# Performance work log

Hardware: AMD Instinct MI355X
Metric: run time of the kernel (lower is better)

## Reference

```python
import jax, jax.numpy as jnp
import numpy as np

N = 100_000
E = 1_000_000
F_IN = 128
F_OUT = 64
NHOP = 2


def _xavier(k, shape, gain=1.414):
    fan_in, fan_out = shape
    std = gain * np.sqrt(2.0 / (fan_in + fan_out))
    return (jax.random.normal(k, shape) * std).astype(jnp.float32)


def setup_inputs() -> dict:
    key = jax.random.key(0)
    ks = jax.random.split(key, 8)
    x = jax.random.normal(ks[0], (N, F_IN), jnp.float32)
    edge_index = jax.random.randint(ks[1], (2, E), 0, N)
    edge_attr = jax.random.uniform(ks[2], (E,), jnp.float32)
    W0 = _xavier(ks[3], (F_IN, F_OUT))
    W1 = _xavier(ks[4], (F_IN, F_OUT))
    b0 = jnp.zeros((F_OUT,), jnp.float32)
    b1 = jnp.zeros((F_OUT,), jnp.float32)
    fc0 = _xavier(ks[5], (F_OUT, 1))
    fc1 = _xavier(ks[6], (F_OUT, 1))
    bf0 = jnp.zeros((1,), jnp.float32)
    bf1 = jnp.zeros((1,), jnp.float32)
    return dict(x=x, edge_index=edge_index, edge_attr=edge_attr,
                W0=W0, b0=b0, W1=W1, b1=b1,
                fc0=fc0, bf0=bf0, fc1=fc1, bf1=bf1)


def _spmm(row, col, val, v, n):
    # (A v)[r] = sum over edges (r -> c) of val * v[c]
    return jax.ops.segment_sum(val[:, None] * v[col], row, num_segments=n)


def _adaptive_enc(y, fc, bf):
    # NodeAdaptiveEncoder (eval mode): relu(y) + sigmoid(y@fc+bf) * min(y, 0)
    g = jax.nn.sigmoid(y @ fc + bf)  # [N, 1]
    return jnp.where(y < 0, 0.0, y) + g * jnp.where(y > 0, 0.0, y)


def reference(x, edge_index, edge_attr, W0, b0, W1, b1, fc0, bf0, fc1, bf1):
    n = x.shape[0]
    row, col = edge_index[0], edge_index[1]
    ones = jnp.ones((n, 1), x.dtype)
    params = [(W0, b0, fc0, bf0), (W1, b1, fc1, bf1)]
    outs = []
    for hop in range(NHOP):
        W, b, fc, bf = params[hop]
        h = x @ W  # [N, F_OUT]
        # identity attention; row_uniform norm of A^(hop+1) factors as
        # (A^(hop+1) h) / (A^(hop+1) 1) -- exact since spspmm sums duplicates.
        agg, deg = h, ones
        for _ in range(hop + 1):
            agg = _spmm(row, col, edge_attr, agg, n)
            deg = _spmm(row, col, edge_attr, deg, n)
        safe_deg = jnp.where(deg > 0, deg, 1.0)
        y = jnp.where(deg > 0, agg / safe_deg, 0.0)  # NaN mask for empty rows
        y = y + b
        outs.append(_adaptive_enc(y, fc, bf))
    return jnp.concatenate(outs, axis=1)  # [N, NHOP * F_OUT]
```

## Files before the change

### kernel.cpp

```cpp
#include <hip/hip_runtime.h>

#define F_IN 128
#define F_ALL 128
#define F_HOP 64

#define RPB_BITS 8
#define RPB 256
#define KB_MAX 512
#define NBLK_BIN 256
#define ECAP 3072

typedef unsigned int uint;
typedef unsigned short ushort;
typedef __attribute__((ext_vector_type(8))) short short8v;
typedef __attribute__((ext_vector_type(4))) float float4v;

__device__ __forceinline__ uint pack_bf16(float lo, float hi) {
    uint ul = __float_as_uint(lo), uh = __float_as_uint(hi);
    ul += 0x7FFFu + ((ul >> 16) & 1u);
    uh += 0x7FFFu + ((uh >> 16) & 1u);
    return (ul >> 16) | (uh & 0xFFFF0000u);
}
__device__ __forceinline__ float bf_lo(uint h) { return __uint_as_float(h << 16); }
__device__ __forceinline__ float bf_hi(uint h) { return __uint_as_float(h & 0xFFFF0000u); }

__global__ __launch_bounds__(256) void gemm_hist_kernel(
    const float* __restrict__ x, const float* __restrict__ W0,
    const float* __restrict__ W1, uint* __restrict__ H2,
    const int* __restrict__ ei, int* __restrict__ bhist,
    int N, int E, int K, int gemmBlocks) {
    __shared__ ushort Wlds[16384];

    if ((int)blockIdx.x >= gemmBlocks) {
        int* h = (int*)Wlds;
        const int hb = blockIdx.x - gemmBlocks;
        for (int i = threadIdx.x; i < K; i += 256) h[i] = 0;
        __syncthreads();
        const int chunk = (E + NBLK_BIN - 1) / NBLK_BIN;
        const int s = hb * chunk;
        const int e = min(s + chunk, E);
        for (int j = s + threadIdx.x; j < e; j += 256)
            atomicAdd(&h[__builtin_nontemporal_load(ei + j) >> RPB_BITS], 1);
        __syncthreads();
        for (int i = threadIdx.x; i < K; i += 256)
            bhist[hb * KB_MAX + i] = h[i];
        return;
    }

    {
        const int t = threadIdx.x;
        #pragma unroll
        for (int i = 0; i < 8; ++i) {
            const int e    = t + 256 * i;
            const int lane = e & 63;
            const int tile = e >> 6;
            const int kt   = tile >> 3;
            const int nt   = tile & 7;
            const int k0   = kt * 32 + (lane >> 4) * 8;
            const int n    = nt * 16 + (lane & 15);
            const float* src = (n < 64) ? (W0 + n) : (W1 + (n - 64));
            float v[8];
            #pragma unroll
            for (int j = 0; j < 8; ++j) v[j] = src[(size_t)(k0 + j) * F_HOP];
            uint4 o;
            o.x = pack_bf16(v[0], v[1]);
            o.y = pack_bf16(v[2], v[3]);
            o.z = pack_bf16(v[4], v[5]);
            o.w = pack_bf16(v[6], v[7]);
            *((uint4*)Wlds + e) = o;
        }
    }
    __syncthreads();

    const int wv   = threadIdx.x >> 6;
    const int lane = threadIdx.x & 63;
    const int rbase = blockIdx.x * 64 + wv * 16;
    if (rbase >= N) return;

    const int m    = lane & 15;
    const int quad = lane >> 4;
    const float* xrow = x + (size_t)(rbase + m) * F_IN + quad * 8;

    float4v acc[8];
    #pragma unroll
    for (int t = 0; t < 8; ++t) acc[t] = (float4v){0.f, 0.f, 0.f, 0.f};

    #pragma unroll
    for (int kt = 0; kt < 4; ++kt) {
        const float4v xa = __builtin_nontemporal_load((const float4v*)(xrow + kt * 32));
        const float4v xb = __builtin_nontemporal_load((const float4v*)(xrow + kt * 32 + 4));
        union { uint4 u; short8v s; } av;
        av.u.x = pack_bf16(xa[0], xa[1]);
        av.u.y = pack_bf16(xa[2], xa[3]);
        av.u.z = pack_bf16(xb[0], xb[1]);
        av.u.w = pack_bf16(xb[2], xb[3]);
        #pragma unroll
        for (int nt = 0; nt < 8; ++nt) {
            union { uint4 u; short8v s; } bv;
            bv.u = *((const uint4*)Wlds + (kt * 8 + nt) * 64 + lane);
            acc[nt] = __builtin_amdgcn_mfma_f32_16x16x32_bf16(av.s, bv.s, acc[nt], 0, 0, 0);
        }
    }

    #pragma unroll
    for (int t = 0; t < 4; ++t) {
        #pragma unroll
        for (int i = 0; i < 4; ++i) {
            const int r = rbase + quad * 4 + i;
            H2[(size_t)r * F_HOP + t * 16 + m] = pack_bf16(acc[t][i], acc[t + 4][i]);
        }
    }
}

__global__ __launch_bounds__(256) void blockscan_kernel(
    int* __restrict__ bhist, int* __restrict__ btot,
    int* __restrict__ rowptr, int E, int N) {
    __shared__ int wsum[4];
    const int b = blockIdx.x;
    const int t = threadIdx.x;
    const int s = bhist[t * KB_MAX + b];
    int v = s;
    #pragma unroll
    for (int d = 1; d < 64; d <<= 1) {
        int u = __shfl_up(v, (unsigned)d, 64);
        if ((t & 63) >= d) v += u;
    }
    if ((t & 63) == 63) wsum[t >> 6] = v;
    __syncthreads();
    int off = 0;
    #pragma unroll
    for (int i = 0; i < 4; ++i) if (i < (t >> 6)) off += wsum[i];
    bhist[t * KB_MAX + b] = off + v - s;
    if (t == 255) btot[b] = off + v;
    if (b == 0 && t == 0) rowptr[N] = E;
}

__global__ __launch_bounds__(256) void bin_kernel(
    const int* __restrict__ ei, const float* __restrict__ ea,
    const int* __restrict__ bloc, const int* __restrict__ btot,
    int2* __restrict__ gbuf, int E, int K) {
    __shared__ int bb[KB_MAX];
    __shared__ int cur[KB_MAX];
    __shared__ int wsum[4];
    const int t = threadIdx.x;
    const int i0 = 2 * t, i1 = 2 * t + 1;
    const int c0 = (i0 < K) ? btot[i0] : 0;
    const int c1 = (i1 < K) ? btot[i1] : 0;
    const int s = c0 + c1;
    int v = s;
    #pragma unroll
    for (int d = 1; d < 64; d <<= 1) {
        int u = __shfl_up(v, (unsigned)d, 64);
        if ((t & 63) >= d) v += u;
    }
    if ((t & 63) == 63) wsum[t >> 6] = v;
    __syncthreads();
    {
        int off = 0;
        #pragma unroll
        for (int i = 0; i < 4; ++i) if (i < (t >> 6)) off += wsum[i];
        const int excl = off + v - s;
        if (i0 < K) bb[i0] = excl;
        if (i1 < K) bb[i1] = excl + c0;
    }
    __syncthreads();
    for (int i = t; i < K; i += 256)
        cur[i] = bb[i] + bloc[blockIdx.x * KB_MAX + i];
    __syncthreads();
    const int chunk = (E + NBLK_BIN - 1) / NBLK_BIN;
    const int s0 = blockIdx.x * chunk;
    const int e0 = min(s0 + chunk, E);
    for (int j = s0 + t; j < e0; j += 256) {
        const int r = __builtin_nontemporal_load(ei + j);
        const int c = __builtin_nontemporal_load(ei + E + j);
        const int vv = __float_as_int(__builtin_nontemporal_load(ea + j));
        const int b = r >> RPB_BITS;
        const int gp = atomicAdd(&cur[b], 1);
        gbuf[gp] = make_int2(c | ((r & (RPB - 1)) << 17), vv);
    }
}

__global__ __launch_bounds__(512) void sort_kernel(
    const int* __restrict__ btot, const int2* __restrict__ gbuf,
    int2* __restrict__ ecv, int* __restrict__ rowptr, int E, int K, int N) {
    __shared__ int2 ebuf[ECAP];
    __shared__ int cnt[RPB];
    __shared__ int bb[KB_MAX + 1];
    __shared__ int wsum[4];
    const int b = blockIdx.x;
    const int t = threadIdx.x;
    const int i0 = 2 * t, i1 = 2 * t + 1;
    const int c0 = (t < 256 && i0 < K) ? btot[i0] : 0;
    const int c1 = (t < 256 && i1 < K) ? btot[i1] : 0;
    const int s = c0 + c1;
    int v = s;
    #pragma unroll
    for (int d = 1; d < 64; d <<= 1) {
        int u = __shfl_up(v, (unsigned)d, 64);
        if ((t & 63) >= d) v += u;
    }
    if (t < 256 && (t & 63) == 63) wsum[t >> 6] = v;
    if (t < RPB) cnt[t] = 0;
    __syncthreads();
    if (t < 256) {
        int off = 0;
        #pragma unroll
        for (int i = 0; i < 4; ++i) if (i < (t >> 6)) off += wsum[i];
        const int excl = off + v - s;
        if (i0 < K) bb[i0] = excl;
        if (i1 < K) bb[i1] = excl + c0;
    }
    if (t == 0) bb[K] = E;
    __syncthreads();
    const int bstart = bb[b], bend = bb[b + 1];
    const int m = bend - bstart;
    const int row0 = b << RPB_BITS;
    for (int j = t; j < m; j += 512) {
        const int2 p = gbuf[bstart + j];
        if (j < ECAP) ebuf[j] = p;
        atomicAdd(&cnt[(p.x >> 17) & (RPB - 1)], 1);
    }
    __syncthreads();
    const int s2 = (t < 256) ? cnt[t] : 0;
    int v2 = s2;
    #pragma unroll
    for (int d = 1; d < 64; d <<= 1) {
        int u = __shfl_up(v2, (unsigned)d, 64);
        if ((t & 63) >= d) v2 += u;
    }
    if (t < 256 && (t & 63) == 63) wsum[t >> 6] = v2;
    __syncthreads();
    int excl2 = 0;
    if (t < 256) {
        int off = 0;
        #pragma unroll
        for (int i = 0; i < 4; ++i) if (i < (t >> 6)) off += wsum[i];
        excl2 = off + v2 - s2;
        const int r0 = row0 + t;
        if (r0 < N) rowptr[r0] = bstart + excl2;
    }
    __syncthreads();
    if (t < 256) cnt[t] = excl2;
    __syncthreads();
    for (int j = t; j < m; j += 512) {
        const int2 p = (j < ECAP) ? ebuf[j] : gbuf[bstart + j];
        const int lr = (p.x >> 17) & (RPB - 1);
        const int pos = atomicAdd(&cnt[lr], 1);
        ecv[bstart + pos] = make_int2(p.x & 0x1FFFF, p.y);
    }
}

__global__ __launch_bounds__(256) void pass1_kernel(
    const int* __restrict__ rowptr, const int2* __restrict__ ecv,
    const uint* __restrict__ H2,
    const float* __restrict__ b0, const float* __restrict__ fc0,
    const float* __restrict__ bf0,
    float* __restrict__ out, ushort* __restrict__ T16,
    float* __restrict__ dg1, int N) {
    const int lane = threadIdx.x & 63;
    const int g    = lane >> 4;
    const int l    = lane & 15;
    const int r = blockIdx.x * 16 + (threadIdx.x >> 6) * 4 + g;
    if (r >= N) return;
    const int f0 = l * 4;
    const uint* __restrict__ H2b = H2 + f0;
    const int jb = rowptr[r], je = rowptr[r + 1];

    float s00 = 0.f, s01 = 0.f, s02 = 0.f, s03 = 0.f;
    float s10 = 0.f, s11 = 0.f, s12 = 0.f, s13 = 0.f;
    float d = 0.f;
    int j = jb;
    for (; j + 4 <= je; j += 4) {
        const int2 e0 = ecv[j], e1 = ecv[j + 1], e2 = ecv[j + 2], e3 = ecv[j + 3];
        const uint4 h0 = *(const uint4*)(H2b + (size_t)e0.x * F_HOP);
        const uint4 h1 = *(const uint4*)(H2b + (size_t)e1.x * F_HOP);
        const uint4 h2 = *(const uint4*)(H2b + (size_t)e2.x * F_HOP);
        const uint4 h3 = *(const uint4*)(H2b + (size_t)e3.x * F_HOP);
        const float v0 = __int_as_float(e0.y), v1 = __int_as_float(e1.y);
        const float v2 = __int_as_float(e2.y), v3 = __int_as_float(e3.y);
        d += (v0 + v1) + (v2 + v3);
        s00 = fmaf(v0, bf_lo(h0.x), s00); s10 = fmaf(v0, bf_hi(h0.x), s10);
        s01 = fmaf(v0, bf_lo(h0.y), s01); s11 = fmaf(v0, bf_hi(h0.y), s11);
        s02 = fmaf(v0, bf_lo(h0.z), s02); s12 = fmaf(v0, bf_hi(h0.z), s12);
        s03 = fmaf(v0, bf_lo(h0.w), s03); s13 = fmaf(v0, bf_hi(h0.w), s13);
        s00 = fmaf(v1, bf_lo(h1.x), s00); s10 = fmaf(v1, bf_hi(h1.x), s10);
        s01 = fmaf(v1, bf_lo(h1.y), s01); s11 = fmaf(v1, bf_hi(h1.y), s11);
        s02 = fmaf(v1, bf_lo(h1.z), s02); s12 = fmaf(v1, bf_hi(h1.z), s12);
        s03 = fmaf(v1, bf_lo(h1.w), s03); s13 = fmaf(v1, bf_hi(h1.w), s13);
        s00 = fmaf(v2, bf_lo(h2.x), s00); s10 = fmaf(v2, bf_hi(h2.x), s10);
        s01 = fmaf(v2, bf_lo(h2.y), s01); s11 = fmaf(v2, bf_hi(h2.y), s11);
        s02 = fmaf(v2, bf_lo(h2.z), s02); s12 = fmaf(v2, bf_hi(h2.z), s12);
        s03 = fmaf(v2, bf_lo(h2.w), s03); s13 = fmaf(v2, bf_hi(h2.w), s13);
        s00 = fmaf(v3, bf_lo(h3.x), s00); s10 = fmaf(v3, bf_hi(h3.x), s10);
        s01 = fmaf(v3, bf_lo(h3.y), s01); s11 = fmaf(v3, bf_hi(h3.y), s11);
        s02 = fmaf(v3, bf_lo(h3.z), s02); s12 = fmaf(v3, bf_hi(h3.z), s12);
        s03 = fmaf(v3, bf_lo(h3.w), s03); s13 = fmaf(v3, bf_hi(h3.w), s13);
    }
    for (; j < je; ++j) {
        const int2 e0 = ecv[j];
        const uint4 h0 = *(const uint4*)(H2b + (size_t)e0.x * F_HOP);
        const float v0 = __int_as_float(e0.y);
        d += v0;
        s00 = fmaf(v0, bf_lo(h0.x), s00); s10 = fmaf(v0, bf_hi(h0.x), s10);
        s01 = fmaf(v0, bf_lo(h0.y), s01); s11 = fmaf(v0, bf_hi(h0.y), s11);
        s02 = fmaf(v0, bf_lo(h0.z), s02); s12 = fmaf(v0, bf_hi(h0.z), s12);
        s03 = fmaf(v0, bf_lo(h0.w), s03); s13 = fmaf(v0, bf_hi(h0.w), s13);
    }

    uint2 tw;
    tw.x = pack_bf16(s10, s11);
    tw.y = pack_bf16(s12, s13);
    *(uint2*)(T16 + (size_t)r * F_HOP + f0) = tw;
    if (l == 0) dg1[r] = d;

    const float inv = (d > 0.f) ? 1.f / d : 0.f;
    const float4 bb = *(const float4*)(b0 + f0);
    const float4 ff = *(const float4*)(fc0 + f0);
    const float y0 = s00 * inv + bb.x;
    const float y1 = s01 * inv + bb.y;
    const float y2 = s02 * inv + bb.z;
    const float y3 = s03 * inv + bb.w;
    float t = y0 * ff.x + y1 * ff.y + y2 * ff.z + y3 * ff.w;
    #pragma unroll
    for (int m = 1; m < 16; m <<= 1) t += __shfl_xor(t, m, 64);
    const float gg = 1.f / (1.f + __expf(-(t + bf0[0])));
    float4v o;
    o[0] = fmaxf(y0, 0.f) + gg * fminf(y0, 0.f);
    o[1] = fmaxf(y1, 0.f) + gg * fminf(y1, 0.f);
    o[2] = fmaxf(y2, 0.f) + gg * fminf(y2, 0.f);
    o[3] = fmaxf(y3, 0.f) + gg * fminf(y3, 0.f);
    __builtin_nontemporal_store(o, (float4v*)(out + (size_t)r * F_ALL + f0));
}

__global__ __launch_bounds__(256) void pass2_kernel(
    const int* __restrict__ rowptr, const int2* __restrict__ ecv,
    const ushort* __restrict__ T16, const float* __restrict__ dg1,
    const float* __restrict__ b1, const float* __restrict__ fc1,
    const float* __restrict__ bf1,
    float* __restrict__ out, int N) {
    const int lane = threadIdx.x & 63;
    const int g    = lane >> 4;
    const int l    = lane & 15;
    const int r = blockIdx.x * 16 + (threadIdx.x >> 6) * 4 + g;
    if (r >= N) return;
    const int f0 = l * 4;
    const ushort* __restrict__ Tb = T16 + f0;
    const int jb = rowptr[r], je = rowptr[r + 1];

    float s0 = 0.f, s1 = 0.f, s2 = 0.f, s3 = 0.f;
    float d2 = 0.f;
    int j = jb;
    for (; j + 4 <= je; j += 4) {
        const int2 e0 = ecv[j], e1 = ecv[j + 1], e2 = ecv[j + 2], e3 = ecv[j + 3];
        const uint2 t0 = *(const uint2*)(Tb + (size_t)e0.x * F_HOP);
        const uint2 t1 = *(const uint2*)(Tb + (size_t)e1.x * F_HOP);
        const uint2 t2 = *(const uint2*)(Tb + (size_t)e2.x * F_HOP);
        const uint2 t3 = *(const uint2*)(Tb + (size_t)e3.x * F_HOP);
        const float g0 = dg1[e0.x], g1 = dg1[e1.x], g2 = dg1[e2.x], g3 = dg1[e3.x];
        const float v0 = __int_as_float(e0.y), v1 = __int_as_float(e1.y);
        const float v2 = __int_as_float(e2.y), v3 = __int_as_float(e3.y);
        d2 = fmaf(v0, g0, d2); d2 = fmaf(v1, g1, d2);
        d2 = fmaf(v2, g2, d2); d2 = fmaf(v3, g3, d2);
        s0 = fmaf(v0, bf_lo(t0.x), s0); s1 = fmaf(v0, bf_hi(t0.x), s1);
        s2 = fmaf(v0, bf_lo(t0.y), s2); s3 = fmaf(v0, bf_hi(t0.y), s3);
        s0 = fmaf(v1, bf_lo(t1.x), s0); s1 = fmaf(v1, bf_hi(t1.x), s1);
        s2 = fmaf(v1, bf_lo(t1.y), s2); s3 = fmaf(v1, bf_hi(t1.y), s3);
        s0 = fmaf(v2, bf_lo(t2.x), s0); s1 = fmaf(v2, bf_hi(t2.x), s1);
        s2 = fmaf(v2, bf_lo(t2.y), s2); s3 = fmaf(v2, bf_hi(t2.y), s3);
        s0 = fmaf(v3, bf_lo(t3.x), s0); s1 = fmaf(v3, bf_hi(t3.x), s1);
        s2 = fmaf(v3, bf_lo(t3.y), s2); s3 = fmaf(v3, bf_hi(t3.y), s3);
    }
    for (; j < je; ++j) {
        const int2 e0 = ecv[j];
        const uint2 t0 = *(const uint2*)(Tb + (size_t)e0.x * F_HOP);
        const float v0 = __int_as_float(e0.y);
        d2 = fmaf(v0, dg1[e0.x], d2);
        s0 = fmaf(v0, bf_lo(t0.x), s0); s1 = fmaf(v0, bf_hi(t0.x), s1);
        s2 = fmaf(v0, bf_lo(t0.y), s2); s3 = fmaf(v0, bf_hi(t0.y), s3);
    }

    const float inv = (d2 > 0.f) ? 1.f / d2 : 0.f;
    const float4 bb = *(const float4*)(b1 + f0);
    const float4 ff = *(const float4*)(fc1 + f0);
    const float y0 = s0 * inv + bb.x;
    const float y1 = s1 * inv + bb.y;
    const float y2 = s2 * inv + bb.z;
    const float y3 = s3 * inv + bb.w;
    float t = y0 * ff.x + y1 * ff.y + y2 * ff.z + y3 * ff.w;
    #pragma unroll
    for (int m = 1; m < 16; m <<= 1) t += __shfl_xor(t, m, 64);
    const float gg = 1.f / (1.f + __expf(-(t + bf1[0])));
    float4v o;
    o[0] = fmaxf(y0, 0.f) + gg * fminf(y0, 0.f);
    o[1] = fmaxf(y1, 0.f) + gg * fminf(y1, 0.f);
    o[2] = fmaxf(y2, 0.f) + gg * fminf(y2, 0.f);
    o[3] = fmaxf(y3, 0.f) + gg * fminf(y3, 0.f);
    __builtin_nontemporal_store(o, (float4v*)(out + (size_t)r * F_ALL + F_HOP + f0));
}

extern "C" void kernel_launch(void* const* d_in, const int* in_sizes, int n_in,
                              void* d_out, int out_size, void* d_ws, size_t ws_size,
                              hipStream_t stream) {
    const float* x   = (const float*)d_in[0];
    const int*   ei  = (const int*)  d_in[1];
    const float* ea  = (const float*)d_in[2];
    const float* W0  = (const float*)d_in[3];
    const float* b0  = (const float*)d_in[4];
    const float* W1  = (const float*)d_in[5];
    const float* b1  = (const float*)d_in[6];
    const float* fc0 = (const float*)d_in[7];
    const float* bf0 = (const float*)d_in[8];
    const float* fc1 = (const float*)d_in[9];
    const float* bf1 = (const float*)d_in[10];
    float* out = (float*)d_out;

    const int N = in_sizes[0] / F_IN;
    const int E = in_sizes[2];
    const int K = (N + RPB - 1) >> RPB_BITS;

    uint*   H2   = (uint*)d_ws;
    ushort* T16  = (ushort*)(H2 + (size_t)N * F_HOP);
    float*  dg1  = (float*)(T16 + (size_t)N * F_HOP);
    int2*   gbuf = (int2*)(dg1 + (size_t)((N + 3) & ~3));
    int2*   ecv  = gbuf + (size_t)E;
    int*    bhist = (int*)(ecv + (size_t)E);
    int*    btot  = bhist + (size_t)NBLK_BIN * KB_MAX;
    int*    rowptr = btot + (KB_MAX + 4);

    const int gemmBlocks = (N + 63) / 64;
    gemm_hist_kernel<<<gemmBlocks + NBLK_BIN, 256, 0, stream>>>(
        x, W0, W1, H2, ei, bhist, N, E, K, gemmBlocks);

    blockscan_kernel<<<K, 256, 0, stream>>>(bhist, btot, rowptr, E, N);
    bin_kernel<<<NBLK_BIN, 256, 0, stream>>>(ei, ea, bhist, btot, gbuf, E, K);
    sort_kernel<<<K, 512, 0, stream>>>(btot, gbuf, ecv, rowptr, E, K, N);

    pass1_kernel<<<(N + 15) / 16, 256, 0, stream>>>(
        rowptr, ecv, H2, b0, fc0, bf0, out, T16, dg1, N);

    pass2_kernel<<<(N + 15) / 16, 256, 0, stream>>>(
        rowptr, ecv, T16, dg1, b1, fc1, bf1, out, N);
}
```

Baseline: 234.9 us.

## Fuse per-bucket row sort into SpMM passes and drop the sort kernel

```diff
diff --git a/kernel.cpp b/kernel.cpp
--- a/kernel.cpp
+++ b/kernel.cpp
@@ -4,11 +4,11 @@
 #define F_ALL 128
 #define F_HOP 64
 
-#define RPB_BITS 8
-#define RPB 256
-#define KB_MAX 512
-#define NBLK_BIN 256
-#define ECAP 3072
+#define RPB_BITS 7
+#define RPB 128
+#define KB_MAX 1024
+#define NBLK_BIN 512
+#define ECAP 2048
 
 typedef unsigned int uint;
 typedef unsigned short ushort;
@@ -112,10 +112,9 @@
     }
 }
 
-__global__ __launch_bounds__(256) void blockscan_kernel(
-    int* __restrict__ bhist, int* __restrict__ btot,
-    int* __restrict__ rowptr, int E, int N) {
-    __shared__ int wsum[4];
+__global__ __launch_bounds__(512) void blockscan_kernel(
+    int* __restrict__ bhist, int* __restrict__ btot) {
+    __shared__ int wsum[8];
     const int b = blockIdx.x;
     const int t = threadIdx.x;
     const int s = bhist[t * KB_MAX + b];
@@ -129,24 +128,25 @@
     __syncthreads();
     int off = 0;
     #pragma unroll
-    for (int i = 0; i < 4; ++i) if (i < (t >> 6)) off += wsum[i];
+    for (int i = 0; i < 8; ++i) if (i < (t >> 6)) off += wsum[i];
     bhist[t * KB_MAX + b] = off + v - s;
-    if (t == 255) btot[b] = off + v;
-    if (b == 0 && t == 0) rowptr[N] = E;
+    if (t == 511) btot[b] = off + v;
 }
 
 __global__ __launch_bounds__(256) void bin_kernel(
     const int* __restrict__ ei, const float* __restrict__ ea,
     const int* __restrict__ bloc, const int* __restrict__ btot,
-    int2* __restrict__ gbuf, int E, int K) {
+    int* __restrict__ bbase_g, int2* __restrict__ gbuf, int E, int K) {
     __shared__ int bb[KB_MAX];
     __shared__ int cur[KB_MAX];
     __shared__ int wsum[4];
     const int t = threadIdx.x;
-    const int i0 = 2 * t, i1 = 2 * t + 1;
-    const int c0 = (i0 < K) ? btot[i0] : 0;
-    const int c1 = (i1 < K) ? btot[i1] : 0;
-    const int s = c0 + c1;
+    const int i0 = 4 * t;
+    const int c0 = (i0     < K) ? btot[i0]     : 0;
+    const int c1 = (i0 + 1 < K) ? btot[i0 + 1] : 0;
+    const int c2 = (i0 + 2 < K) ? btot[i0 + 2] : 0;
+    const int c3 = (i0 + 3 < K) ? btot[i0 + 3] : 0;
+    const int s = c0 + c1 + c2 + c3;
     int v = s;
     #pragma unroll
     for (int d = 1; d < 64; d <<= 1) {
@@ -160,10 +160,16 @@
         #pragma unroll
         for (int i = 0; i < 4; ++i) if (i < (t >> 6)) off += wsum[i];
         const int excl = off + v - s;
-        if (i0 < K) bb[i0] = excl;
-        if (i1 < K) bb[i1] = excl + c0;
-    }
-    __syncthreads();
+        if (i0     < K) bb[i0]     = excl;
+        if (i0 + 1 < K) bb[i0 + 1] = excl + c0;
+        if (i0 + 2 < K) bb[i0 + 2] = excl + c0 + c1;
+        if (i0 + 3 < K) bb[i0 + 3] = excl + c0 + c1 + c2;
+    }
+    __syncthreads();
+    if (blockIdx.x == 0) {
+        for (int i = t; i < K; i += 256) bbase_g[i] = bb[i];
+        if (t == 0) bbase_g[K] = E;
+    }
     for (int i = t; i < K; i += 256)
         cur[i] = bb[i] + bloc[blockIdx.x * KB_MAX + i];
     __syncthreads();
@@ -180,222 +186,288 @@
     }
 }
 
-__global__ __launch_bounds__(512) void sort_kernel(
-    const int* __restrict__ btot, const int2* __restrict__ gbuf,
-    int2* __restrict__ ecv, int* __restrict__ rowptr, int E, int K, int N) {
-    __shared__ int2 ebuf[ECAP];
-    __shared__ int cnt[RPB];
-    __shared__ int bb[KB_MAX + 1];
-    __shared__ int wsum[4];
-    const int b = blockIdx.x;
-    const int t = threadIdx.x;
-    const int i0 = 2 * t, i1 = 2 * t + 1;
-    const int c0 = (t < 256 && i0 < K) ? btot[i0] : 0;
-    const int c1 = (t < 256 && i1 < K) ? btot[i1] : 0;
-    const int s = c0 + c1;
-    int v = s;
-    #pragma unroll
-    for (int d = 1; d < 64; d <<= 1) {
-        int u = __shfl_up(v, (unsigned)d, 64);
-        if ((t & 63) >= d) v += u;
-    }
-    if (t < 256 && (t & 63) == 63) wsum[t >> 6] = v;
-    if (t < RPB) cnt[t] = 0;
-    __syncthreads();
-    if (t < 256) {
-        int off = 0;
-        #pragma unroll
-        for (int i = 0; i < 4; ++i) if (i < (t >> 6)) off += wsum[i];
-        const int excl = off + v - s;
-        if (i0 < K) bb[i0] = excl;
-        if (i1 < K) bb[i1] = excl + c0;
-    }
-    if (t == 0) bb[K] = E;
-    __syncthreads();
-    const int bstart = bb[b], bend = bb[b + 1];
-    const int m = bend - bstart;
-    const int row0 = b << RPB_BITS;
-    for (int j = t; j < m; j += 512) {
-        const int2 p = gbuf[bstart + j];
-        if (j < ECAP) ebuf[j] = p;
-        atomicAdd(&cnt[(p.x >> 17) & (RPB - 1)], 1);
-    }
-    __syncthreads();
-    const int s2 = (t < 256) ? cnt[t] : 0;
-    int v2 = s2;
-    #pragma unroll
-    for (int d = 1; d < 64; d <<= 1) {
-        int u = __shfl_up(v2, (unsigned)d, 64);
-        if ((t & 63) >= d) v2 += u;
-    }
-    if (t < 256 && (t & 63) == 63) wsum[t >> 6] = v2;
-    __syncthreads();
-    int excl2 = 0;
-    if (t < 256) {
-        int off = 0;
-        #pragma unroll
-        for (int i = 0; i < 4; ++i) if (i < (t >> 6)) off += wsum[i];
-        excl2 = off + v2 - s2;
-        const int r0 = row0 + t;
-        if (r0 < N) rowptr[r0] = bstart + excl2;
-    }
-    __syncthreads();
-    if (t < 256) cnt[t] = excl2;
-    __syncthreads();
-    for (int j = t; j < m; j += 512) {
-        const int2 p = (j < ECAP) ? ebuf[j] : gbuf[bstart + j];
-        const int lr = (p.x >> 17) & (RPB - 1);
-        const int pos = atomicAdd(&cnt[lr], 1);
-        ecv[bstart + pos] = make_int2(p.x & 0x1FFFF, p.y);
-    }
-}
-
-__global__ __launch_bounds__(256) void pass1_kernel(
-    const int* __restrict__ rowptr, const int2* __restrict__ ecv,
+__global__ __launch_bounds__(512) void pass1_kernel(
+    const int* __restrict__ bbase, const int2* __restrict__ gbuf,
     const uint* __restrict__ H2,
     const float* __restrict__ b0, const float* __restrict__ fc0,
     const float* __restrict__ bf0,
     float* __restrict__ out, ushort* __restrict__ T16,
     float* __restrict__ dg1, int N) {
-    const int lane = threadIdx.x & 63;
-    const int g    = lane >> 4;
-    const int l    = lane & 15;
-    const int r = blockIdx.x * 16 + (threadIdx.x >> 6) * 4 + g;
-    if (r >= N) return;
+    __shared__ int2 ebuf[ECAP];
+    __shared__ int cnt[RPB];
+    __shared__ int rp[RPB + 1];
+    __shared__ int wsum2[2];
+    const int t = threadIdx.x;
+    const int b = blockIdx.x;
+    const int bstart = bbase[b];
+    const int m = bbase[b + 1] - bstart;
+    const int mc = (m < ECAP) ? m : ECAP;
+    const int row0 = b << RPB_BITS;
+
+    if (t < RPB) cnt[t] = 0;
+    __syncthreads();
+    for (int j = t; j < mc; j += 512) {
+        const int2 p = gbuf[bstart + j];
+        ebuf[j] = p;
+        atomicAdd(&cnt[(p.x >> 17) & (RPB - 1)], 1);
+    }
+    __syncthreads();
+    int sv = 0, vv = 0;
+    if (t < RPB) {
+        sv = cnt[t];
+        vv = sv;
+        #pragma unroll
+        for (int d = 1; d < 64; d <<= 1) {
+            int u = __shfl_up(vv, (unsigned)d, 64);
+            if ((t & 63) >= d) vv += u;
+        }
+        if ((t & 63) == 63) wsum2[t >> 6] = vv;
+    }
+    __syncthreads();
+    if (t < RPB) rp[t] = ((t >= 64) ? wsum2[0] : 0) + vv - sv;
+    if (t == 0) rp[RPB] = mc;
+    __syncthreads();
+    if (t < RPB) cnt[t] = rp[t];
+    __syncthreads();
+    int2 pr[4]; int pp[4]; bool pvld[4];
+    #pragma unroll
+    for (int k2 = 0; k2 < 4; ++k2) {
+        const int j = t + 512 * k2;
+        pvld[k2] = (j < mc);
+        if (pvld[k2]) {
+            pr[k2] = ebuf[j];
+            pp[k2] = atomicAdd(&cnt[(pr[k2].x >> 17) & (RPB - 1)], 1);
+        }
+    }
+    __syncthreads();
+    #pragma unroll
+    for (int k2 = 0; k2 < 4; ++k2)
+        if (pvld[k2]) ebuf[pp[k2]] = pr[k2];
+    __syncthreads();
+
+    const int l  = t & 15;
+    const int g  = t >> 4;
     const int f0 = l * 4;
     const uint* __restrict__ H2b = H2 + f0;
-    const int jb = rowptr[r], je = rowptr[r + 1];
-
-    float s00 = 0.f, s01 = 0.f, s02 = 0.f, s03 = 0.f;
-    float s10 = 0.f, s11 = 0.f, s12 = 0.f, s13 = 0.f;
-    float d = 0.f;
-    int j = jb;
-    for (; j + 4 <= je; j += 4) {
-        const int2 e0 = ecv[j], e1 = ecv[j + 1], e2 = ecv[j + 2], e3 = ecv[j + 3];
-        const uint4 h0 = *(const uint4*)(H2b + (size_t)e0.x * F_HOP);
-        const uint4 h1 = *(const uint4*)(H2b + (size_t)e1.x * F_HOP);
-        const uint4 h2 = *(const uint4*)(H2b + (size_t)e2.x * F_HOP);
-        const uint4 h3 = *(const uint4*)(H2b + (size_t)e3.x * F_HOP);
-        const float v0 = __int_as_float(e0.y), v1 = __int_as_float(e1.y);
-        const float v2 = __int_as_float(e2.y), v3 = __int_as_float(e3.y);
-        d += (v0 + v1) + (v2 + v3);
-        s00 = fmaf(v0, bf_lo(h0.x), s00); s10 = fmaf(v0, bf_hi(h0.x), s10);
-        s01 = fmaf(v0, bf_lo(h0.y), s01); s11 = fmaf(v0, bf_hi(h0.y), s11);
-        s02 = fmaf(v0, bf_lo(h0.z), s02); s12 = fmaf(v0, bf_hi(h0.z), s12);
-        s03 = fmaf(v0, bf_lo(h0.w), s03); s13 = fmaf(v0, bf_hi(h0.w), s13);
-        s00 = fmaf(v1, bf_lo(h1.x), s00); s10 = fmaf(v1, bf_hi(h1.x), s10);
-        s01 = fmaf(v1, bf_lo(h1.y), s01); s11 = fmaf(v1, bf_hi(h1.y), s11);
-        s02 = fmaf(v1, bf_lo(h1.z), s02); s12 = fmaf(v1, bf_hi(h1.z), s12);
-        s03 = fmaf(v1, bf_lo(h1.w), s03); s13 = fmaf(v1, bf_hi(h1.w), s13);
-        s00 = fmaf(v2, bf_lo(h2.x), s00); s10 = fmaf(v2, bf_hi(h2.x), s10);
-        s01 = fmaf(v2, bf_lo(h2.y), s01); s11 = fmaf(v2, bf_hi(h2.y), s11);
-        s02 = fmaf(v2, bf_lo(h2.z), s02); s12 = fmaf(v2, bf_hi(h2.z), s12);
-        s03 = fmaf(v2, bf_lo(h2.w), s03); s13 = fmaf(v2, bf_hi(h2.w), s13);
-        s00 = fmaf(v3, bf_lo(h3.x), s00); s10 = fmaf(v3, bf_hi(h3.x), s10);
-        s01 = fmaf(v3, bf_lo(h3.y), s01); s11 = fmaf(v3, bf_hi(h3.y), s11);
-        s02 = fmaf(v3, bf_lo(h3.z), s02); s12 = fmaf(v3, bf_hi(h3.z), s12);
-        s03 = fmaf(v3, bf_lo(h3.w), s03); s13 = fmaf(v3, bf_hi(h3.w), s13);
-    }
-    for (; j < je; ++j) {
-        const int2 e0 = ecv[j];
-        const uint4 h0 = *(const uint4*)(H2b + (size_t)e0.x * F_HOP);
-        const float v0 = __int_as_float(e0.y);
-        d += v0;
-        s00 = fmaf(v0, bf_lo(h0.x), s00); s10 = fmaf(v0, bf_hi(h0.x), s10);
-        s01 = fmaf(v0, bf_lo(h0.y), s01); s11 = fmaf(v0, bf_hi(h0.y), s11);
-        s02 = fmaf(v0, bf_lo(h0.z), s02); s12 = fmaf(v0, bf_hi(h0.z), s12);
-        s03 = fmaf(v0, bf_lo(h0.w), s03); s13 = fmaf(v0, bf_hi(h0.w), s13);
-    }
-
-    uint2 tw;
-    tw.x = pack_bf16(s10, s11);
-    tw.y = pack_bf16(s12, s13);
-    *(uint2*)(T16 + (size_t)r * F_HOP + f0) = tw;
-    if (l == 0) dg1[r] = d;
-
-    const float inv = (d > 0.f) ? 1.f / d : 0.f;
-    const float4 bb = *(const float4*)(b0 + f0);
-    const float4 ff = *(const float4*)(fc0 + f0);
-    const float y0 = s00 * inv + bb.x;
-    const float y1 = s01 * inv + bb.y;
-    const float y2 = s02 * inv + bb.z;
-    const float y3 = s03 * inv + bb.w;
-    float t = y0 * ff.x + y1 * ff.y + y2 * ff.z + y3 * ff.w;
-    #pragma unroll
-    for (int m = 1; m < 16; m <<= 1) t += __shfl_xor(t, m, 64);
-    const float gg = 1.f / (1.f + __expf(-(t + bf0[0])));
-    float4v o;
-    o[0] = fmaxf(y0, 0.f) + gg * fminf(y0, 0.f);
-    o[1] = fmaxf(y1, 0.f) + gg * fminf(y1, 0.f);
-    o[2] = fmaxf(y2, 0.f) + gg * fminf(y2, 0.f);
-    o[3] = fmaxf(y3, 0.f) + gg * fminf(y3, 0.f);
-    __builtin_nontemporal_store(o, (float4v*)(out + (size_t)r * F_ALL + f0));
-}
-
-__global__ __launch_bounds__(256) void pass2_kernel(
-    const int* __restrict__ rowptr, const int2* __restrict__ ecv,
+
+    for (int k = 0; k < 4; ++k) {
+        const int lr = g * 4 + k;
+        const int r = row0 + lr;
+        if (r >= N) break;
+        const int jb = rp[lr], je = rp[lr + 1];
+
+        float s00 = 0.f, s01 = 0.f, s02 = 0.f, s03 = 0.f;
+        float s10 = 0.f, s11 = 0.f, s12 = 0.f, s13 = 0.f;
+        float d = 0.f;
+        int j = jb;
+        for (; j + 4 <= je; j += 4) {
+            const int2 e0 = ebuf[j], e1 = ebuf[j + 1], e2 = ebuf[j + 2], e3 = ebuf[j + 3];
+            const uint4 h0 = *(const uint4*)(H2b + (size_t)(e0.x & 0x1FFFF) * F_HOP);
+            const uint4 h1 = *(const uint4*)(H2b + (size_t)(e1.x & 0x1FFFF) * F_HOP);
+            const uint4 h2 = *(const uint4*)(H2b + (size_t)(e2.x & 0x1FFFF) * F_HOP);
+            const uint4 h3 = *(const uint4*)(H2b + (size_t)(e3.x & 0x1FFFF) * F_HOP);
+            const float v0 = __int_as_float(e0.y), v1 = __int_as_float(e1.y);
+            const float v2 = __int_as_float(e2.y), v3 = __int_as_float(e3.y);
+            d += (v0 + v1) + (v2 + v3);
+            s00 = fmaf(v0, bf_lo(h0.x), s00); s10 = fmaf(v0, bf_hi(h0.x), s10);
+            s01 = fmaf(v0, bf_lo(h0.y), s01); s11 = fmaf(v0, bf_hi(h0.y), s11);
+            s02 = fmaf(v0, bf_lo(h0.z), s02); s12 = fmaf(v0, bf_hi(h0.z), s12);
+            s03 = fmaf(v0, bf_lo(h0.w), s03); s13 = fmaf(v0, bf_hi(h0.w), s13);
+            s00 = fmaf(v1, bf_lo(h1.x), s00); s10 = fmaf(v1, bf_hi(h1.x), s10);
+            s01 = fmaf(v1, bf_lo(h1.y), s01); s11 = fmaf(v1, bf_hi(h1.y), s11);
+            s02 = fmaf(v1, bf_lo(h1.z), s02); s12 = fmaf(v1, bf_hi(h1.z), s12);
+            s03 = fmaf(v1, bf_lo(h1.w), s03); s13 = fmaf(v1, bf_hi(h1.w), s13);
+            s00 = fmaf(v2, bf_lo(h2.x), s00); s10 = fmaf(v2, bf_hi(h2.x), s10);
+            s01 = fmaf(v2, bf_lo(h2.y), s01); s11 = fmaf(v2, bf_hi(h2.y), s11);
+            s02 = fmaf(v2, bf_lo(h2.z), s02); s12 = fmaf(v2, bf_hi(h2.z), s12);
+            s03 = fmaf(v2, bf_lo(h2.w), s03); s13 = fmaf(v2, bf_hi(h2.w), s13);
+            s00 = fmaf(v3, bf_lo(h3.x), s00); s10 = fmaf(v3, bf_hi(h3.x), s10);
+            s01 = fmaf(v3, bf_lo(h3.y), s01); s11 = fmaf(v3, bf_hi(h3.y), s11);
+            s02 = fmaf(v3, bf_lo(h3.z), s02); s12 = fmaf(v3, bf_hi(h3.z), s12);
+            s03 = fmaf(v3, bf_lo(h3.w), s03); s13 = fmaf(v3, bf_hi(h3.w), s13);
+        }
+        for (; j < je; ++j) {
+            const int2 e0 = ebuf[j];
+            const uint4 h0 = *(const uint4*)(H2b + (size_t)(e0.x & 0x1FFFF) * F_HOP);
+            const float v0 = __int_as_float(e0.y);
+            d += v0;
+            s00 = fmaf(v0, bf_lo(h0.x), s00); s10 = fmaf(v0, bf_hi(h0.x), s10);
+            s01 = fmaf(v0, bf_lo(h0.y), s01); s11 = fmaf(v0, bf_hi(h0.y), s11);
+            s02 = fmaf(v0, bf_lo(h0.z), s02); s12 = fmaf(v0, bf_hi(h0.z), s12);
+            s03 = fmaf(v0, bf_lo(h0.w), s03); s13 = fmaf(v0, bf_hi(h0.w), s13);
+        }
+        for (int j2 = ECAP; j2 < m; ++j2) {
+            const int2 p = gbuf[bstart + j2];
+            if (((p.x >> 17) & (RPB - 1)) == lr) {
+                const uint4 h0 = *(const uint4*)(H2b + (size_t)(p.x & 0x1FFFF) * F_HOP);
+                const float v0 = __int_as_float(p.y);
+                d += v0;
+                s00 = fmaf(v0, bf_lo(h0.x), s00); s10 = fmaf(v0, bf_hi(h0.x), s10);
+                s01 = fmaf(v0, bf_lo(h0.y), s01); s11 = fmaf(v0, bf_hi(h0.y), s11);
+                s02 = fmaf(v0, bf_lo(h0.z), s02); s12 = fmaf(v0, bf_hi(h0.z), s12);
+                s03 = fmaf(v0, bf_lo(h0.w), s03); s13 = fmaf(v0, bf_hi(h0.w), s13);
+            }
+        }
+
+        uint2 tw;
+        tw.x = pack_bf16(s10, s11);
+        tw.y = pack_bf16(s12, s13);
+        *(uint2*)(T16 + (size_t)r * F_HOP + f0) = tw;
+        if (l == 0) dg1[r] = d;
+
+        const float inv = (d > 0.f) ? 1.f / d : 0.f;
+        const float4 bb4 = *(const float4*)(b0 + f0);
+        const float4 ff = *(const float4*)(fc0 + f0);
+        const float y0 = s00 * inv + bb4.x;
+        const float y1 = s01 * inv + bb4.y;
+        const float y2 = s02 * inv + bb4.z;
+        const float y3 = s03 * inv + bb4.w;
+        float tt = y0 * ff.x + y1 * ff.y + y2 * ff.z + y3 * ff.w;
+        #pragma unroll
+        for (int mm = 1; mm < 16; mm <<= 1) tt += __shfl_xor(tt, mm, 64);
+        const float gg = 1.f / (1.f + __expf(-(tt + bf0[0])));
+        float4v o;
+        o[0] = fmaxf(y0, 0.f) + gg * fminf(y0, 0.f);
+        o[1] = fmaxf(y1, 0.f) + gg * fminf(y1, 0.f);
+        o[2] = fmaxf(y2, 0.f) + gg * fminf(y2, 0.f);
+        o[3] = fmaxf(y3, 0.f) + gg * fminf(y3, 0.f);
+        __builtin_nontemporal_store(o, (float4v*)(out + (size_t)r * F_ALL + f0));
+    }
+}
+
+__global__ __launch_bounds__(512) void pass2_kernel(
+    const int* __restrict__ bbase, const int2* __restrict__ gbuf,
     const ushort* __restrict__ T16, const float* __restrict__ dg1,
     const float* __restrict__ b1, const float* __restrict__ fc1,
     const float* __restrict__ bf1,
     float* __restrict__ out, int N) {
-    const int lane = threadIdx.x & 63;
-    const int g    = lane >> 4;
-    const int l    = lane & 15;
-    const int r = blockIdx.x * 16 + (threadIdx.x >> 6) * 4 + g;
-    if (r >= N) return;
+    __shared__ int2 ebuf[ECAP];
+    __shared__ int cnt[RPB];
+    __shared__ int rp[RPB + 1];
+    __shared__ int wsum2[2];
+    const int t = threadIdx.x;
+    const int b = blockIdx.x;
+    const int bstart = bbase[b];
+    const int m = bbase[b + 1] - bstart;
+    const int mc = (m < ECAP) ? m : ECAP;
+    const int row0 = b << RPB_BITS;
+
+    if (t < RPB) cnt[t] = 0;
+    __syncthreads();
+    for (int j = t; j < mc; j += 512) {
+        const int2 p = gbuf[bstart + j];
+        ebuf[j] = p;
+        atomicAdd(&cnt[(p.x >> 17) & (RPB - 1)], 1);
+    }
+    __syncthreads();
+    int sv = 0, vv = 0;
+    if (t < RPB) {
+        sv = cnt[t];
+        vv = sv;
+        #pragma unroll
+        for (int d = 1; d < 64; d <<= 1) {
+            int u = __shfl_up(vv, (unsigned)d, 64);
+            if ((t & 63) >= d) vv += u;
+        }
+        if ((t & 63) == 63) wsum2[t >> 6] = vv;
+    }
+    __syncthreads();
+    if (t < RPB) rp[t] = ((t >= 64) ? wsum2[0] : 0) + vv - sv;
+    if (t == 0) rp[RPB] = mc;
+    __syncthreads();
+    if (t < RPB) cnt[t] = rp[t];
+    __syncthreads();
+    int2 pr[4]; int pp[4]; bool pvld[4];
+    #pragma unroll
+    for (int k2 = 0; k2 < 4; ++k2) {
+        const int j = t + 512 * k2;
+        pvld[k2] = (j < mc);
+        if (pvld[k2]) {
+            pr[k2] = ebuf[j];
+            pp[k2] = atomicAdd(&cnt[(pr[k2].x >> 17) & (RPB - 1)], 1);
+        }
+    }
+    __syncthreads();
+    #pragma unroll
+    for (int k2 = 0; k2 < 4; ++k2)
+        if (pvld[k2]) ebuf[pp[k2]] = pr[k2];
+    __syncthreads();
+
+    const int l  = t & 15;
+    const int g  = t >> 4;
     const int f0 = l * 4;
     const ushort* __restrict__ Tb = T16 + f0;
-    const int jb = rowptr[r], je = rowptr[r + 1];
-
-    float s0 = 0.f, s1 = 0.f, s2 = 0.f, s3 = 0.f;
-    float d2 = 0.f;
-    int j = jb;
-    for (; j + 4 <= je; j += 4) {
-        const int2 e0 = ecv[j], e1 = ecv[j + 1], e2 = ecv[j + 2], e3 = ecv[j + 3];
-        const uint2 t0 = *(const uint2*)(Tb + (size_t)e0.x * F_HOP);
-        const uint2 t1 = *(const uint2*)(Tb + (size_t)e1.x * F_HOP);
-        const uint2 t2 = *(const uint2*)(Tb + (size_t)e2.x * F_HOP);
-        const uint2 t3 = *(const uint2*)(Tb + (size_t)e3.x * F_HOP);
-        const float g0 = dg1[e0.x], g1 = dg1[e1.x], g2 = dg1[e2.x], g3 = dg1[e3.x];
-        const float v0 = __int_as_float(e0.y), v1 = __int_as_float(e1.y);
-        const float v2 = __int_as_float(e2.y), v3 = __int_as_float(e3.y);
-        d2 = fmaf(v0, g0, d2); d2 = fmaf(v1, g1, d2);
-        d2 = fmaf(v2, g2, d2); d2 = fmaf(v3, g3, d2);
-        s0 = fmaf(v0, bf_lo(t0.x), s0); s1 = fmaf(v0, bf_hi(t0.x), s1);
-        s2 = fmaf(v0, bf_lo(t0.y), s2); s3 = fmaf(v0, bf_hi(t0.y), s3);
-        s0 = fmaf(v1, bf_lo(t1.x), s0); s1 = fmaf(v1, bf_hi(t1.x), s1);
-        s2 = fmaf(v1, bf_lo(t1.y), s2); s3 = fmaf(v1, bf_hi(t1.y), s3);
-        s0 = fmaf(v2, bf_lo(t2.x), s0); s1 = fmaf(v2, bf_hi(t2.x), s1);
-        s2 = fmaf(v2, bf_lo(t2.y), s2); s3 = fmaf(v2, bf_hi(t2.y), s3);
-        s0 = fmaf(v3, bf_lo(t3.x), s0); s1 = fmaf(v3, bf_hi(t3.x), s1);
-        s2 = fmaf(v3, bf_lo(t3.y), s2); s3 = fmaf(v3, bf_hi(t3.y), s3);
-    }
-    for (; j < je; ++j) {
-        const int2 e0 = ecv[j];
-        const uint2 t0 = *(const uint2*)(Tb + (size_t)e0.x * F_HOP);
-        const float v0 = __int_as_float(e0.y);
-        d2 = fmaf(v0, dg1[e0.x], d2);
-        s0 = fmaf(v0, bf_lo(t0.x), s0); s1 = fmaf(v0, bf_hi(t0.x), s1);
-        s2 = fmaf(v0, bf_lo(t0.y), s2); s3 = fmaf(v0, bf_hi(t0.y), s3);
-    }
-
-    const float inv = (d2 > 0.f) ? 1.f / d2 : 0.f;
-    const float4 bb = *(const float4*)(b1 + f0);
-    const float4 ff = *(const float4*)(fc1 + f0);
-    const float y0 = s0 * inv + bb.x;
-    const float y1 = s1 * inv + bb.y;
-    const float y2 = s2 * inv + bb.z;
-    const float y3 = s3 * inv + bb.w;
-    float t = y0 * ff.x + y1 * ff.y + y2 * ff.z + y3 * ff.w;
-    #pragma unroll
-    for (int m = 1; m < 16; m <<= 1) t += __shfl_xor(t, m, 64);
-    const float gg = 1.f / (1.f + __expf(-(t + bf1[0])));
-    float4v o;
-    o[0] = fmaxf(y0, 0.f) + gg * fminf(y0, 0.f);
-    o[1] = fmaxf(y1, 0.f) + gg * fminf(y1, 0.f);
-    o[2] = fmaxf(y2, 0.f) + gg * fminf(y2, 0.f);
-    o[3] = fmaxf(y3, 0.f) + gg * fminf(y3, 0.f);
-    __builtin_nontemporal_store(o, (float4v*)(out + (size_t)r * F_ALL + F_HOP + f0));
+
+    for (int k = 0; k < 4; ++k) {
+        const int lr = g * 4 + k;
+        const int r = row0 + lr;
+        if (r >= N) break;
+        const int jb = rp[lr], je = rp[lr + 1];
+
+        float s0 = 0.f, s1 = 0.f, s2 = 0.f, s3 = 0.f;
+        float d2 = 0.f;
+        int j = jb;
+        for (; j + 4 <= je; j += 4) {
+            const int2 e0 = ebuf[j], e1 = ebuf[j + 1], e2 = ebuf[j + 2], e3 = ebuf[j + 3];
+            const int c0i = e0.x & 0x1FFFF, c1i = e1.x & 0x1FFFF;
+            const int c2i = e2.x & 0x1FFFF, c3i = e3.x & 0x1FFFF;
+            const uint2 t0 = *(const uint2*)(Tb + (size_t)c0i * F_HOP);
+            const uint2 t1 = *(const uint2*)(Tb + (size_t)c1i * F_HOP);
+            const uint2 t2 = *(const uint2*)(Tb + (size_t)c2i * F_HOP);
+            const uint2 t3 = *(const uint2*)(Tb + (size_t)c3i * F_HOP);
+            const float g0 = dg1[c0i], g1 = dg1[c1i], g2 = dg1[c2i], g3 = dg1[c3i];
+            const float v0 = __int_as_float(e0.y), v1 = __int_as_float(e1.y);
+            const float v2 = __int_as_float(e2.y), v3 = __int_as_float(e3.y);
+            d2 = fmaf(v0, g0, d2); d2 = fmaf(v1, g1, d2);
+            d2 = fmaf(v2, g2, d2); d2 = fmaf(v3, g3, d2);
+            s0 = fmaf(v0, bf_lo(t0.x), s0); s1 = fmaf(v0, bf_hi(t0.x), s1);
+            s2 = fmaf(v0, bf_lo(t0.y), s2); s3 = fmaf(v0, bf_hi(t0.y), s3);
+            s0 = fmaf(v1, bf_lo(t1.x), s0); s1 = fmaf(v1, bf_hi(t1.x), s1);
+            s2 = fmaf(v1, bf_lo(t1.y), s2); s3 = fmaf(v1, bf_hi(t1.y), s3);
+            s0 = fmaf(v2, bf_lo(t2.x), s0); s1 = fmaf(v2, bf_hi(t2.x), s1);
+            s2 = fmaf(v2, bf_lo(t2.y), s2); s3 = fmaf(v2, bf_hi(t2.y), s3);
+            s0 = fmaf(v3, bf_lo(t3.x), s0); s1 = fmaf(v3, bf_hi(t3.x), s1);
+            s2 = fmaf(v3, bf_lo(t3.y), s2); s3 = fmaf(v3, bf_hi(t3.y), s3);
+        }
+        for (; j < je; ++j) {
+            const int2 e0 = ebuf[j];
+            const int c0i = e0.x & 0x1FFFF;
+            const uint2 t0 = *(const uint2*)(Tb + (size_t)c0i * F_HOP);
+            const float v0 = __int_as_float(e0.y);
+            d2 = fmaf(v0, dg1[c0i], d2);
+            s0 = fmaf(v0, bf_lo(t0.x), s0); s1 = fmaf(v0, bf_hi(t0.x), s1);
+            s2 = fmaf(v0, bf_lo(t0.y), s2); s3 = fmaf(v0, bf_hi(t0.y), s3);
+        }
+        for (int j2 = ECAP; j2 < m; ++j2) {
+            const int2 p = gbuf[bstart + j2];
+            if (((p.x >> 17) & (RPB - 1)) == lr) {
+                const int c0i = p.x & 0x1FFFF;
+                const uint2 t0 = *(const uint2*)(Tb + (size_t)c0i * F_HOP);
+                const float v0 = __int_as_float(p.y);
+                d2 = fmaf(v0, dg1[c0i], d2);
+                s0 = fmaf(v0, bf_lo(t0.x), s0); s1 = fmaf(v0, bf_hi(t0.x), s1);
+                s2 = fmaf(v0, bf_lo(t0.y), s2); s3 = fmaf(v0, bf_hi(t0.y), s3);
+            }
+        }
+
+        const float inv = (d2 > 0.f) ? 1.f / d2 : 0.f;
+        const float4 bb4 = *(const float4*)(b1 + f0);
+        const float4 ff = *(const float4*)(fc1 + f0);
+        const float y0 = s0 * inv + bb4.x;
+        const float y1 = s1 * inv + bb4.y;
+        const float y2 = s2 * inv + bb4.z;
+        const float y3 = s3 * inv + bb4.w;
+        float tt = y0 * ff.x + y1 * ff.y + y2 * ff.z + y3 * ff.w;
+        #pragma unroll
+        for (int mm = 1; mm < 16; mm <<= 1) tt += __shfl_xor(tt, mm, 64);
+        const float gg = 1.f / (1.f + __expf(-(tt + bf1[0])));
+        float4v o;
+        o[0] = fmaxf(y0, 0.f) + gg * fminf(y0, 0.f);
+        o[1] = fmaxf(y1, 0.f) + gg * fminf(y1, 0.f);
+        o[2] = fmaxf(y2, 0.f) + gg * fminf(y2, 0.f);
+        o[3] = fmaxf(y3, 0.f) + gg * fminf(y3, 0.f);
+        __builtin_nontemporal_store(o, (float4v*)(out + (size_t)r * F_ALL + F_HOP + f0));
+    }
 }
 
 extern "C" void kernel_launch(void* const* d_in, const int* in_sizes, int n_in,
@@ -422,22 +494,20 @@
     ushort* T16  = (ushort*)(H2 + (size_t)N * F_HOP);
     float*  dg1  = (float*)(T16 + (size_t)N * F_HOP);
     int2*   gbuf = (int2*)(dg1 + (size_t)((N + 3) & ~3));
-    int2*   ecv  = gbuf + (size_t)E;
-    int*    bhist = (int*)(ecv + (size_t)E);
+    int*    bhist = (int*)(gbuf + (size_t)E);
     int*    btot  = bhist + (size_t)NBLK_BIN * KB_MAX;
-    int*    rowptr = btot + (KB_MAX + 4);
+    int*    bbase = btot + (KB_MAX + 4);
 
     const int gemmBlocks = (N + 63) / 64;
     gemm_hist_kernel<<<gemmBlocks + NBLK_BIN, 256, 0, stream>>>(
         x, W0, W1, H2, ei, bhist, N, E, K, gemmBlocks);
 
-    blockscan_kernel<<<K, 256, 0, stream>>>(bhist, btot, rowptr, E, N);
-    bin_kernel<<<NBLK_BIN, 256, 0, stream>>>(ei, ea, bhist, btot, gbuf, E, K);
-    sort_kernel<<<K, 512, 0, stream>>>(btot, gbuf, ecv, rowptr, E, K, N);
-
-    pass1_kernel<<<(N + 15) / 16, 256, 0, stream>>>(
-        rowptr, ecv, H2, b0, fc0, bf0, out, T16, dg1, N);
-
-    pass2_kernel<<<(N + 15) / 16, 256, 0, stream>>>(
-        rowptr, ecv, T16, dg1, b1, fc1, bf1, out, N);
-}
+    blockscan_kernel<<<K, 512, 0, stream>>>(bhist, btot);
+    bin_kernel<<<NBLK_BIN, 256, 0, stream>>>(ei, ea, bhist, btot, bbase, gbuf, E, K);
+
+    pass1_kernel<<<K, 512, 0, stream>>>(
+        bbase, gbuf, H2, b0, fc0, bf0, out, T16, dg1, N);
+
+    pass2_kernel<<<K, 512, 0, stream>>>(
+        bbase, gbuf, T16, dg1, b1, fc1, bf1, out, N);
+}
```

Result: slower. 240.5 us (+2.4%).
